# Optimization experiments

Measured on AMD Instinct MI355X. Metric: run time of the kernel, lower is better.

## Reference

```python
import jax, jax.numpy as jnp
import numpy as np

# Static block node counts (src of layer l has N[l] nodes, dst has N[l+1])
N = [100000, 50000, 25000, 12500]
E = [750000, 250000, 125000]
D = 128          # in_feats == n_hidden
E_PAIR = 10000   # pos/neg pair-graph edges
BN_EPS = 1e-5


def setup_inputs() -> dict:
    key = jax.random.key(0)
    ks = jax.random.split(key, 32)
    inp = {}
    inp['x'] = jax.random.normal(ks[0], (N[0], D), dtype=jnp.float32)
    for l in range(3):
        inp[f'src{l}'] = jax.random.randint(ks[1 + 2 * l], (E[l],), 0, N[l], dtype=jnp.int32)
        inp[f'dst{l}'] = jax.random.randint(ks[2 + 2 * l], (E[l],), 0, N[l + 1], dtype=jnp.int32)
    inp['perm'] = jax.random.permutation(ks[7], N[0]).astype(jnp.int32)
    inp['pos_src'] = jax.random.randint(ks[8], (E_PAIR,), 0, N[3], dtype=jnp.int32)
    inp['pos_dst'] = jax.random.randint(ks[9], (E_PAIR,), 0, N[3], dtype=jnp.int32)
    inp['neg_src'] = jax.random.randint(ks[10], (E_PAIR,), 0, N[3], dtype=jnp.int32)
    inp['neg_dst'] = jax.random.randint(ks[11], (E_PAIR,), 0, N[3], dtype=jnp.int32)
    s = 1.0 / np.sqrt(D)
    ki = 12
    for l in range(3):
        inp[f'Wself{l}'] = jax.random.normal(ks[ki], (D, D), dtype=jnp.float32) * s; ki += 1
        inp[f'Wneigh{l}'] = jax.random.normal(ks[ki], (D, D), dtype=jnp.float32) * s; ki += 1
        inp[f'b{l}'] = jnp.zeros((D,), dtype=jnp.float32)
    for l in range(2):
        inp[f'gamma{l}'] = jnp.ones((D,), dtype=jnp.float32)
        inp[f'beta{l}'] = jnp.zeros((D,), dtype=jnp.float32)
    inp['disc_W'] = jax.random.uniform(ks[ki], (D, D), dtype=jnp.float32, minval=-s, maxval=s); ki += 1
    inp['pW1'] = jax.random.normal(ks[ki], (D, D), dtype=jnp.float32) * s; ki += 1
    inp['pb1'] = jnp.zeros((D,), dtype=jnp.float32)
    inp['pW2'] = jax.random.normal(ks[ki], (D, D), dtype=jnp.float32) * s; ki += 1
    inp['pb2'] = jnp.zeros((D,), dtype=jnp.float32)
    inp['pW3'] = jax.random.normal(ks[ki], (D, 1), dtype=jnp.float32) * s; ki += 1
    inp['pb3'] = jnp.zeros((1,), dtype=jnp.float32)
    return inp


def _sage(h, src, dst, n_dst, Wself, Wneigh, b):
    # DGL SAGEConv('mean'): fc_self(h_dst) + fc_neigh(mean over in-neighbors)
    agg = jax.ops.segment_sum(h[src], dst, num_segments=n_dst)          # [n_dst, D]
    deg = jax.ops.segment_sum(jnp.ones(src.shape, h.dtype), dst, num_segments=n_dst)
    mean = agg / jnp.clip(deg, 1.0)[:, None]
    return h[:n_dst] @ Wself + mean @ Wneigh + b


def _bn(h, g, b):
    m = h.mean(0)
    v = h.var(0)
    return g * (h - m) * jax.lax.rsqrt(v + BN_EPS) + b


def _encode(h, blocks, params):
    for l in range(3):
        src, dst, n_dst = blocks[l]
        Ws, Wn, b, g, be = params[l]
        h = _sage(h, src, dst, n_dst, Ws, Wn, b)
        if l != 2:
            h = jax.nn.relu(_bn(h, g, be))  # dropout rate 0
    return h


def reference(x, src0, dst0, src1, dst1, src2, dst2, perm,
              pos_src, pos_dst, neg_src, neg_dst,
              Wself0, Wneigh0, b0, Wself1, Wneigh1, b1, Wself2, Wneigh2, b2,
              gamma0, beta0, gamma1, beta1, disc_W,
              pW1, pb1, pW2, pb2, pW3, pb3):
    blocks = [(src0, dst0, N[1]), (src1, dst1, N[2]), (src2, dst2, N[3])]
    params = [(Wself0, Wneigh0, b0, gamma0, beta0),
              (Wself1, Wneigh1, b1, gamma1, beta1),
              (Wself2, Wneigh2, b2, None, None)]
    positive = _encode(x, blocks, params)          # [N3, D]
    negative = _encode(x[perm], blocks, params)    # corruption: permuted features
    summary = jax.nn.sigmoid(positive.mean(0))     # [D]
    ws = disc_W @ summary                          # [D]
    pos = positive @ ws                            # [N3]
    neg = negative @ ws
    l1 = jnp.mean(jax.nn.softplus(-pos))           # BCEWithLogits vs ones
    l2 = jnp.mean(jax.nn.softplus(neg))            # BCEWithLogits vs zeros

    def predictor(z):
        z = jax.nn.relu(z @ pW1 + pb1)
        z = jax.nn.relu(z @ pW2 + pb2)
        return z @ pW3 + pb3

    h_pos = predictor(positive[pos_src] * positive[pos_dst])  # [E_PAIR, 1]
    h_neg = predictor(positive[neg_src] * positive[neg_dst])
    return h_pos, h_neg, l1 + l2
```

## Files before the change

kernel.cpp:

```cpp
#include <hip/hip_runtime.h>
#include <hip/hip_bf16.h>

#define DD 128
#define BN_EPS 1e-5f
#define NBLK 160

typedef __hip_bfloat16 bf16;
typedef __attribute__((ext_vector_type(8))) short short8;
typedef __attribute__((ext_vector_type(4))) float f32x4;

__device__ __forceinline__ float b2f(unsigned short u) {
    union { float f; unsigned int i; } x; x.i = ((unsigned int)u) << 16; return x.f;
}
__device__ __forceinline__ unsigned short f2bs(float v) {
    bf16 h = __float2bfloat16(v);
    return *(unsigned short*)&h;
}

__global__ void detect_dtype(const unsigned int* __restrict__ x, int* __restrict__ flag) {
    __shared__ int s[256];
    int t = threadIdx.x;
    unsigned int u = x[t];
    unsigned int e = (u >> 7) & 0xFFu;
    s[t] = ((e >= 90u && e <= 140u) || ((u & 0xFFFFu) == 0u)) ? 1 : 0;
    __syncthreads();
    for (int off = 128; off > 0; off >>= 1) { if (t < off) s[t] += s[t + off]; __syncthreads(); }
    if (t == 0) *flag = (s[0] >= 128) ? 1 : 0;
}

struct CvtTable {
    const void* src[20];
    int off[20];
    int n[20];
    int total;
};
__global__ __launch_bounds__(256) void cvt_all(CvtTable tab, float* __restrict__ wsf,
                                               const int* __restrict__ flagp) {
    int i = blockIdx.x * 256 + threadIdx.x;
    if (i >= tab.total) return;
    int k = 0;
    while (i >= tab.n[k]) { i -= tab.n[k]; ++k; }
    float v;
    if (*flagp) v = b2f(((const unsigned short*)tab.src[k])[i]);
    else        v = ((const float*)tab.src[k])[i];
    wsf[tab.off[k] + i] = v;
}

struct WfAll {
    const float* W1[5];
    const float* W2[5];
    unsigned short* dst[5];
    int KS[5];
    int start[5];
    int total;
};
__global__ __launch_bounds__(256) void wfrag_all(WfAll w) {
    int t = blockIdx.x * 256 + threadIdx.x;
    if (t >= w.total) return;
    int k = 0;
    while (k < 4 && t >= w.start[k + 1]) ++k;
    int lt = t - w.start[k];
    int KS = w.KS[k];
    int lane = lt & 63;
    int ks = (lt >> 6) % KS;
    int ct = lt / (KS * 64);
    int n = ct * 16 + (lane & 15);
    unsigned short v[8];
#pragma unroll
    for (int j = 0; j < 8; ++j) {
        int kk = ks * 32 + ((lane >> 4) & 3) * 8 + j;
        float wv = (kk < 128) ? w.W1[k][kk * DD + n] : w.W2[k][(kk - 128) * DD + n];
        v[j] = f2bs(wv);
    }
    *(uint4*)&w.dst[k][(size_t)lt * 8] = *(uint4*)v;
}

__global__ __launch_bounds__(256) void hist_win(
    const int* __restrict__ d0, int e0, const int* __restrict__ d1, int e1,
    const int* __restrict__ d2, int e2, int* __restrict__ hist) {
    int stride = gridDim.x * 256;
    int t0 = blockIdx.x * 256 + threadIdx.x;
    for (int w = 0; w < 4; ++w) {
        int dlo = w * 12500, dhi = dlo + 12500;
        for (int e = t0; e < e0; e += stride) {
            int d = d0[e];
            if (d >= dlo && d < dhi) atomicAdd(&hist[d], 1);
        }
    }
    for (int e = t0; e < e1; e += stride) atomicAdd(&hist[50000 + d1[e]], 1);
    for (int e = t0; e < e2; e += stride) atomicAdd(&hist[75000 + d2[e]], 1);
}

__global__ __launch_bounds__(256) void scan_bsum(const int* __restrict__ cnt, int n,
                                                 int* __restrict__ bsums) {
    __shared__ int sm[256];
    int t = threadIdx.x, b = blockIdx.x;
    int i4 = b * 256 + t;
    int local = 0;
    if (i4 * 4 < n) { int4 v = ((const int4*)cnt)[i4]; local = v.x + v.y + v.z + v.w; }
    sm[t] = local;
    __syncthreads();
    for (int off = 128; off > 0; off >>= 1) { if (t < off) sm[t] += sm[t + off]; __syncthreads(); }
    if (t == 0) bsums[b] = sm[0];
}
__global__ void scan_bscan(int* __restrict__ bsums, int nb, int* __restrict__ rowptr_n) {
    __shared__ int wsum[4];
    int t = threadIdx.x, lane = t & 63, w = t >> 6;
    int v = (t < nb) ? bsums[t] : 0;
    int inc = v;
    for (int off = 1; off < 64; off <<= 1) {
        int u = __shfl_up(inc, off, 64);
        if (lane >= off) inc += u;
    }
    if (lane == 63) wsum[w] = inc;
    __syncthreads();
    int wo = 0;
    for (int i = 0; i < w; ++i) wo += wsum[i];
    if (t < nb) bsums[t] = wo + inc - v;
    if (t == 255) *rowptr_n = wo + inc;
}
__global__ __launch_bounds__(256) void scan_apply(const int* __restrict__ cnt, int n,
                                                  const int* __restrict__ bsums,
                                                  int* __restrict__ rowptr) {
    __shared__ int wsum[4];
    int t = threadIdx.x, b = blockIdx.x, lane = t & 63, w = t >> 6;
    int i4 = b * 256 + t;
    int4 v = {0, 0, 0, 0};
    bool valid = (i4 * 4 < n);
    if (valid) v = ((const int4*)cnt)[i4];
    int local = v.x + v.y + v.z + v.w;
    int inc = local;
    for (int off = 1; off < 64; off <<= 1) {
        int u = __shfl_up(inc, off, 64);
        if (lane >= off) inc += u;
    }
    if (lane == 63) wsum[w] = inc;
    __syncthreads();
    int wo = 0;
    for (int i = 0; i < w; ++i) wo += wsum[i];
    if (valid) {
        int acc = bsums[b] + wo + inc - local;
        int base = i4 * 4;
        rowptr[base + 0] = acc; acc += v.x;
        rowptr[base + 1] = acc; acc += v.y;
        rowptr[base + 2] = acc; acc += v.z;
        rowptr[base + 3] = acc;
    }
}

__global__ __launch_bounds__(256) void csr_fill_win(
    const int* __restrict__ s0, const int* __restrict__ d0, int e0,
    const int* __restrict__ s1, const int* __restrict__ d1, int e1,
    const int* __restrict__ s2, const int* __restrict__ d2, int e2,
    const int* __restrict__ rpAll, int* __restrict__ cur, int* __restrict__ eid) {
    int stride = gridDim.x * 256;
    int t0 = blockIdx.x * 256 + threadIdx.x;
    for (int w = 0; w < 4; ++w) {
        int dlo = w * 12500, dhi = dlo + 12500;
        for (int e = t0; e < e0; e += stride) {
            int d = d0[e];
            if (d >= dlo && d < dhi)
                eid[rpAll[d] + atomicAdd(&cur[d], 1)] = s0[e];
        }
    }
    for (int e = t0; e < e1; e += stride) {
        int gd = 50000 + d1[e];
        eid[rpAll[gd] + atomicAdd(&cur[gd], 1)] = s1[e];
    }
    for (int e = t0; e < e2; e += stride) {
        int gd = 75000 + d2[e];
        eid[rpAll[gd] + atomicAdd(&cur[gd], 1)] = s2[e];
    }
}

__global__ __launch_bounds__(256) void gather2(
    const void* __restrict__ hvP, const void* __restrict__ hvN,
    const int* __restrict__ flagp,
    const int* __restrict__ permP, const int* __restrict__ permN,
    const float* __restrict__ scP, const float* __restrict__ shP,
    const float* __restrict__ scN, const float* __restrict__ shN,
    const int* __restrict__ rowptr, const int* __restrict__ eid,
    int N, int nRows, unsigned short* __restrict__ out)
{
    int row = blockIdx.x * 4 + (threadIdx.x >> 6);
    int lane = threadIdx.x & 63;
    if (row >= nRows) return;
    int half = row >= N;
    int d = half ? row - N : row;
    const void* hv = half ? hvN : hvP;
    const int* perm = half ? permN : permP;
    const float* sc = half ? scN : scP;
    const float* sh = half ? shN : shP;
    int i0 = rowptr[d], i1 = rowptr[d + 1];
    int abf = flagp ? *flagp : 1;
    bool bn = (sc != nullptr);
    float c0 = 1.0f, c1 = 1.0f, h0 = 0.0f, h1 = 0.0f;
    if (bn) { c0 = sc[lane * 2]; c1 = sc[lane * 2 + 1]; h0 = sh[lane * 2]; h1 = sh[lane * 2 + 1]; }

#define XF0(v) (bn ? fmaxf(c0 * (v) + h0, 0.0f) : (v))
#define XF1(v) (bn ? fmaxf(c1 * (v) + h1, 0.0f) : (v))
    float a0x = 0, a0y = 0, a1x = 0, a1y = 0, a2x = 0, a2y = 0, a3x = 0, a3y = 0;
    int i = i0;
    if (abf) {
        const unsigned short* h = (const unsigned short*)hv;
        for (; i + 4 <= i1; i += 4) {
            int s0 = eid[i], s1 = eid[i + 1], s2 = eid[i + 2], s3 = eid[i + 3];
            if (perm) { s0 = perm[s0]; s1 = perm[s1]; s2 = perm[s2]; s3 = perm[s3]; }
            ushort2 v0 = *(const ushort2*)&h[(size_t)s0 * DD + lane * 2];
            ushort2 v1 = *(const ushort2*)&h[(size_t)s1 * DD + lane * 2];
            ushort2 v2 = *(const ushort2*)&h[(size_t)s2 * DD + lane * 2];
            ushort2 v3 = *(const ushort2*)&h[(size_t)s3 * DD + lane * 2];
            a0x += XF0(b2f(v0.x)); a0y += XF1(b2f(v0.y));
            a1x += XF0(b2f(v1.x)); a1y += XF1(b2f(v1.y));
            a2x += XF0(b2f(v2.x)); a2y += XF1(b2f(v2.y));
            a3x += XF0(b2f(v3.x)); a3y += XF1(b2f(v3.y));
        }
        for (; i < i1; ++i) {
            int s = eid[i];
            if (perm) s = perm[s];
            ushort2 v = *(const ushort2*)&h[(size_t)s * DD + lane * 2];
            a0x += XF0(b2f(v.x)); a0y += XF1(b2f(v.y));
        }
    } else {
        const float* h = (const float*)hv;
        for (; i + 4 <= i1; i += 4) {
            int s0 = eid[i], s1 = eid[i + 1], s2 = eid[i + 2], s3 = eid[i + 3];
            if (perm) { s0 = perm[s0]; s1 = perm[s1]; s2 = perm[s2]; s3 = perm[s3]; }
            float2 v0 = *(const float2*)&h[(size_t)s0 * DD + lane * 2];
            float2 v1 = *(const float2*)&h[(size_t)s1 * DD + lane * 2];
            float2 v2 = *(const float2*)&h[(size_t)s2 * DD + lane * 2];
            float2 v3 = *(const float2*)&h[(size_t)s3 * DD + lane * 2];
            a0x += XF0(v0.x); a0y += XF1(v0.y);
            a1x += XF0(v1.x); a1y += XF1(v1.y);
            a2x += XF0(v2.x); a2y += XF1(v2.y);
            a3x += XF0(v3.x); a3y += XF1(v3.y);
        }
        for (; i < i1; ++i) {
            int s = eid[i];
            if (perm) s = perm[s];
            float2 v = *(const float2*)&h[(size_t)s * DD + lane * 2];
            a0x += XF0(v.x); a0y += XF1(v.y);
        }
    }
#undef XF0
#undef XF1
    float rd = 1.0f / fmaxf((float)(i1 - i0), 1.0f);
    ushort2 o;
    o.x = f2bs((a0x + a1x + a2x + a3x) * rd);
    o.y = f2bs((a0y + a1y + a2y + a3y) * rd);
    *(ushort2*)&out[(size_t)row * DD + lane * 2] = o;
}

#define ALD 264
__global__ __launch_bounds__(256) void mfma_gemm(
    const void* __restrict__ A1v, const int* __restrict__ flagp,
    const int* __restrict__ gather,
    const float* __restrict__ bnSc, const float* __restrict__ bnSh,
    const unsigned short* __restrict__ A2,
    const uint4* __restrict__ wfrag, const float* __restrict__ bias,
    unsigned short* __restrict__ out, int Mc, int relu,
    float* __restrict__ PSo, float* __restrict__ PQo)
{
    __shared__ unsigned short As[64 * ALD];
    __shared__ float sds[256];
    const int tid = threadIdx.x;
    const int rb = blockIdx.x * 64;
    const int abf = flagp ? *flagp : 1;
    const int KS = A2 ? 8 : 4;

    {
        int r = tid >> 2, cs = (tid & 3) * 32;
        int gr = rb + r;
        unsigned short* dst = &As[r * ALD + cs];
        if (gr < Mc) {
            int ar = gather ? gather[gr] : gr;
            if (abf) {
                if (bnSc) {
                    const unsigned short* s = (const unsigned short*)A1v + (size_t)ar * DD + cs;
#pragma unroll
                    for (int i = 0; i < 32; ++i) {
                        float v = b2f(s[i]);
                        v = fmaxf(bnSc[cs + i] * v + bnSh[cs + i], 0.0f);
                        dst[i] = f2bs(v);
                    }
                } else {
                    const uint4* s = (const uint4*)((const unsigned short*)A1v + (size_t)ar * DD + cs);
                    uint4* dv = (uint4*)dst;
#pragma unroll
                    for (int i = 0; i < 4; ++i) dv[i] = s[i];
                }
            } else {
                const float* s = (const float*)A1v + (size_t)ar * DD + cs;
#pragma unroll
                for (int i = 0; i < 32; ++i) dst[i] = f2bs(s[i]);
            }
            if (A2) {
                const uint4* s2 = (const uint4*)(A2 + (size_t)gr * DD + cs);
                uint4* d2 = (uint4*)(dst + 128);
#pragma unroll
                for (int i = 0; i < 4; ++i) d2[i] = s2[i];
            }
        } else {
            uint4 z = {0, 0, 0, 0};
            uint4* dv = (uint4*)dst;
#pragma unroll
            for (int i = 0; i < 4; ++i) dv[i] = z;
            if (A2) {
                uint4* d2 = (uint4*)(dst + 128);
#pragma unroll
                for (int i = 0; i < 4; ++i) d2[i] = z;
            }
        }
    }
    if (PSo) { sds[tid] = 0.0f; }
    __syncthreads();

    const int w = tid >> 6, lane = tid & 63;
    const int m0 = w * 16;
    f32x4 acc[8] = {};

    for (int ks = 0; ks < KS; ++ks) {
        short8 a = *(const short8*)&As[(m0 + (lane & 15)) * ALD + ks * 32 + ((lane >> 4) & 3) * 8];
#pragma unroll
        for (int ct = 0; ct < 8; ++ct) {
            uint4 braw = wfrag[(ct * KS + ks) * 64 + lane];
            short8 b = *(short8*)&braw;
            acc[ct] = __builtin_amdgcn_mfma_f32_16x16x32_bf16(a, b, acc[ct], 0, 0, 0);
        }
    }

#pragma unroll
    for (int ct = 0; ct < 8; ++ct) {
        int col = ct * 16 + (lane & 15);
        float bv = bias[col];
        float sv = 0.0f, sq = 0.0f;
#pragma unroll
        for (int r = 0; r < 4; ++r) {
            int grow = rb + m0 + ((lane >> 4) & 3) * 4 + r;
            float v = acc[ct][r] + bv;
            if (relu) v = fmaxf(v, 0.0f);
            if (grow < Mc) {
                out[(size_t)grow * DD + col] = f2bs(v);
                sv += v; sq += v * v;
            }
        }
        if (PSo) {
            sv += __shfl_down(sv, 32, 64); sv += __shfl_down(sv, 16, 64);
            sq += __shfl_down(sq, 32, 64); sq += __shfl_down(sq, 16, 64);
            if (lane < 16) {
                atomicAdd(&sds[ct * 16 + lane], sv);
                atomicAdd(&sds[128 + ct * 16 + lane], sq);
            }
        }
    }
    if (PSo) {
        __syncthreads();
        if (tid < 128) {
            PSo[blockIdx.x * 128 + tid] = sds[tid];
            PQo[blockIdx.x * 128 + tid] = sds[128 + tid];
        }
    }
}

__global__ __launch_bounds__(256) void p2bn_fast(
    const float* __restrict__ PSa, const float* __restrict__ PQa,
    float* __restrict__ sca, float* __restrict__ sha,
    const float* __restrict__ PSb, const float* __restrict__ PQb,
    float* __restrict__ scb, float* __restrict__ shb,
    int nb, int M,
    const float* __restrict__ gamma, const float* __restrict__ beta)
{
    int tensor = blockIdx.x >> 7, col = blockIdx.x & 127;
    const float* PS = tensor ? PSb : PSa;
    const float* PQ = tensor ? PQb : PQa;
    float* sc = tensor ? scb : sca;
    float* sh = tensor ? shb : sha;
    __shared__ float sS[256], sQ[256];
    int t = threadIdx.x;
    float s = 0.0f, q = 0.0f;
    for (int b = t; b < nb; b += 256) {
        s += PS[b * 128 + col];
        q += PQ[b * 128 + col];
    }
    sS[t] = s; sQ[t] = q;
    __syncthreads();
    for (int off = 128; off > 0; off >>= 1) {
        if (t < off) { sS[t] += sS[t + off]; sQ[t] += sQ[t + off]; }
        __syncthreads();
    }
    if (t == 0) {
        float m = sS[0] / (float)M;
        float var = fmaxf(sQ[0] / (float)M - m * m, 0.0f);
        float inv = rsqrtf(var + BN_EPS);
        float g = gamma[col];
        sc[col] = g * inv;
        sh[col] = beta[col] - g * m * inv;
    }
}

__global__ __launch_bounds__(256) void colreduce(const float* __restrict__ PS, int nb,
                                                 float* __restrict__ out) {
    __shared__ float sS[256];
    int col = blockIdx.x;
    int t = threadIdx.x;
    float s = 0.0f;
    for (int b = t; b < nb; b += 256) s += PS[b * 128 + col];
    sS[t] = s;
    __syncthreads();
    for (int off = 128; off > 0; off >>= 1) { if (t < off) sS[t] += sS[t + off]; __syncthreads(); }
    if (t == 0) out[col] = sS[0];
}

__global__ void make_ws(const float* __restrict__ colsum, const float* __restrict__ discW,
                        float* __restrict__ wsv, int M) {
    __shared__ float s[128];
    int t = threadIdx.x;
    s[t] = 1.0f / (1.0f + expf(-(colsum[t] / (float)M)));
    __syncthreads();
    float acc = 0.0f;
#pragma unroll
    for (int j = 0; j < 128; ++j) acc += discW[t * 128 + j] * s[j];
    wsv[t] = acc;
}

__global__ __launch_bounds__(256) void loss_partial(
    const unsigned short* __restrict__ P, const unsigned short* __restrict__ Ng,
    const float* __restrict__ wsv, float* __restrict__ lossP, float* __restrict__ lossN, int M)
{
    __shared__ float sP[4], sN[4];
    int lane = threadIdx.x & 63;
    int wave = threadIdx.x >> 6;
    int gw = blockIdx.x * 4 + wave;
    int nw = gridDim.x * 4;
    float w0 = wsv[lane], w1 = wsv[lane + 64];
    float accP = 0.0f, accN = 0.0f;
    for (int row = gw; row < 2 * M; row += nw) {
        const unsigned short* base = (row < M) ? &P[(size_t)row * DD]
                                               : &Ng[(size_t)(row - M) * DD];
        float a = b2f(base[lane]) * w0 + b2f(base[lane + 64]) * w1;
#pragma unroll
        for (int off = 32; off > 0; off >>= 1) a += __shfl_down(a, off, 64);
        if (lane == 0) {
            float x = (row < M) ? -a : a;
            float sp = fmaxf(x, 0.0f) + log1pf(expf(-fabsf(x)));
            if (row < M) accP += sp; else accN += sp;
        }
    }
    if (lane == 0) { sP[wave] = accP; sN[wave] = accN; }
    __syncthreads();
    if (threadIdx.x == 0) {
        lossP[blockIdx.x] = sP[0] + sP[1] + sP[2] + sP[3];
        lossN[blockIdx.x] = sN[0] + sN[1] + sN[2] + sN[3];
    }
}

__global__ void write_loss(const float* __restrict__ lossP, const float* __restrict__ lossN,
                           void* __restrict__ outv, int M, const int* __restrict__ flagp) {
    __shared__ float s[256];
    int t = threadIdx.x;
    s[t] = (t < NBLK) ? (lossP[t] + lossN[t]) : 0.0f;
    __syncthreads();
    for (int off = 128; off > 0; off >>= 1) { if (t < off) s[t] += s[t + off]; __syncthreads(); }
    if (t == 0) {
        float v = s[0] / (float)M;
        if (*flagp) ((bf16*)outv)[20000] = __float2bfloat16(v);
        else        ((float*)outv)[20000] = v;
    }
}

__global__ __launch_bounds__(256) void pair_mult(
    const unsigned short* __restrict__ P,
    const int* __restrict__ ps, const int* __restrict__ pd,
    const int* __restrict__ ns, const int* __restrict__ nd,
    unsigned short* __restrict__ Z, int nPair) {
    int i = blockIdx.x * 2 + (threadIdx.x >> 7);
    int f = threadIdx.x & 127;
    if (i >= 2 * nPair) return;
    int a = (i < nPair) ? ps[i] : ns[i - nPair];
    int b = (i < nPair) ? pd[i] : nd[i - nPair];
    float v = b2f(P[(size_t)a * DD + f]) * b2f(P[(size_t)b * DD + f]);
    Z[(size_t)i * DD + f] = f2bs(v);
}

__global__ __launch_bounds__(256) void final_mv(
    const unsigned short* __restrict__ ZB, const float* __restrict__ pW3,
    const float* __restrict__ pb3,
    void* __restrict__ outv, int nRows, const int* __restrict__ flagp) {
    int row = blockIdx.x * 4 + (threadIdx.x >> 6);
    int lane = threadIdx.x & 63;
    if (row >= nRows) return;
    float a = b2f(ZB[(size_t)row * DD + lane]) * pW3[lane]
            + b2f(ZB[(size_t)row * DD + lane + 64]) * pW3[lane + 64];
#pragma unroll
    for (int off = 32; off > 0; off >>= 1) a += __shfl_down(a, off, 64);
    if (lane == 0) {
        float v = a + pb3[0];
        if (*flagp) ((bf16*)outv)[row] = __float2bfloat16(v);
        else        ((float*)outv)[row] = v;
    }
}

extern "C" void kernel_launch(void* const* d_in, const int* in_sizes, int n_in,
                              void* d_out, int out_size, void* d_ws, size_t ws_size,
                              hipStream_t stream)
{
    const void* x      = d_in[0];
    const int* srcA[3] = {(const int*)d_in[1], (const int*)d_in[3], (const int*)d_in[5]};
    const int* dstA[3] = {(const int*)d_in[2], (const int*)d_in[4], (const int*)d_in[6]};
    const int* perm    = (const int*)d_in[7];
    const int* pos_src = (const int*)d_in[8];
    const int* pos_dst = (const int*)d_in[9];
    const int* neg_src = (const int*)d_in[10];
    const int* neg_dst = (const int*)d_in[11];

    const int N1 = 50000, N2 = 25000, N3 = 12500;
    const int E[3] = {750000, 250000, 125000};
    const int EP = 10000;
    const int NCAT = 87500;

    float* wsf = (float*)d_ws;
    int*   wsi = (int*)d_ws;
    int*   flagp = wsi;
    float* lossP = wsf + 64;
    float* lossN = wsf + 224;
    float* wsvec = wsf + 512;
    float* scP0 = wsf + 640;  float* shP0 = wsf + 768;
    float* scN0 = wsf + 896;  float* shN0 = wsf + 1024;
    float* scP1 = wsf + 1152; float* shP1 = wsf + 1280;
    float* scN1 = wsf + 1408; float* shN1 = wsf + 1536;
    int*   bsums = wsi + 1664;
    float* colsum = wsf + 1920;
    float* PSP = wsf + 2048;
    float* PQP = wsf + 102400;
    float* PSN = wsf + 202752;
    float* PQN = wsf + 303104;
    int* histAll = wsi + 403456;
    int* curAll  = wsi + 491008;
    int* rpAll   = wsi + 578560;
    int* eidAll  = wsi + 666112;
    const size_t WfB = 1791232;
    float* WS[3] = {wsf + WfB, wsf + WfB + 32896, wsf + WfB + 65792};
    float* WN[3] = {wsf + WfB + 16384, wsf + WfB + 49280, wsf + WfB + 82176};
    float* BV[3] = {wsf + WfB + 32768, wsf + WfB + 65664, wsf + WfB + 98560};
    float* G0  = wsf + WfB + 98688;  float* BE0 = wsf + WfB + 98816;
    float* G1  = wsf + WfB + 98944;  float* BE1 = wsf + WfB + 99072;
    float* DW  = wsf + WfB + 99200;
    float* PW1 = wsf + WfB + 115584; float* PB1 = wsf + WfB + 131968;
    float* PW2 = wsf + WfB + 132096; float* PB2 = wsf + WfB + 148480;
    float* PW3 = wsf + WfB + 148608; float* PB3 = wsf + WfB + 148736;
    unsigned short* wfragL[3] = {(unsigned short*)(wsf + 1940480),
                                 (unsigned short*)(wsf + 1956864),
                                 (unsigned short*)(wsf + 1973248)};
    unsigned short* wfragP[2] = {(unsigned short*)(wsf + 1989632),
                                 (unsigned short*)(wsf + 1997824)};
    unsigned short* PF  = (unsigned short*)(wsf + 2006016);
    unsigned short* NF  = (unsigned short*)(wsf + 2806016);
    unsigned short* H2P = (unsigned short*)(wsf + 3606016);
    unsigned short* H2N = (unsigned short*)(wsf + 5206016);
    unsigned short* H1P = (unsigned short*)(wsf + 6806016);
    unsigned short* H1N = (unsigned short*)(wsf + 10006016);
    unsigned short* AGG = (unsigned short*)(wsf + 13206016);
    unsigned short* Z  = H1P;
    unsigned short* ZA = H1N;
    unsigned short* ZB = H1N + (size_t)1280000 * 2;

    detect_dtype<<<1, 256, 0, stream>>>((const unsigned int*)x, flagp);
    CvtTable tab;
    const int widx[20] = {12,13,14, 15,16,17, 18,19,20, 21,22,23,24, 25, 26,27, 28,29, 30,31};
    float* wdst[20] = {WS[0],WN[0],BV[0], WS[1],WN[1],BV[1], WS[2],WN[2],BV[2],
                       G0,BE0,G1,BE1, DW, PW1,PB1, PW2,PB2, PW3,PB3};
    const int wn[20] = {16384,16384,128, 16384,16384,128, 16384,16384,128,
                        128,128,128,128, 16384, 16384,128, 16384,128, 128,1};
    int tot = 0;
    for (int k = 0; k < 20; ++k) {
        tab.src[k] = d_in[widx[k]];
        tab.off[k] = (int)(wdst[k] - wsf);
        tab.n[k] = wn[k];
        tot += wn[k];
    }
    tab.total = tot;
    cvt_all<<<(tot + 255) / 256, 256, 0, stream>>>(tab, wsf, flagp);

    hipMemsetAsync(histAll, 0, (size_t)(2 * NCAT + 128) * 4, stream);
    hist_win<<<512, 256, 0, stream>>>(dstA[0], E[0], dstA[1], E[1], dstA[2], E[2], histAll);
    {
        int nb = (NCAT / 4 + 255) / 256;
        scan_bsum<<<nb, 256, 0, stream>>>(histAll, NCAT, bsums);
        scan_bscan<<<1, 256, 0, stream>>>(bsums, nb, rpAll + NCAT);
        scan_apply<<<nb, 256, 0, stream>>>(histAll, NCAT, bsums, rpAll);
    }
    csr_fill_win<<<512, 256, 0, stream>>>(
        srcA[0], dstA[0], E[0], srcA[1], dstA[1], E[1], srcA[2], dstA[2], E[2],
        rpAll, curAll, eidAll);

    WfAll wa;
    wa.W1[0] = WS[0]; wa.W2[0] = WN[0]; wa.dst[0] = wfragL[0]; wa.KS[0] = 8; wa.start[0] = 0;
    wa.W1[1] = WS[1]; wa.W2[1] = WN[1]; wa.dst[1] = wfragL[1]; wa.KS[1] = 8; wa.start[1] = 4096;
    wa.W1[2] = WS[2]; wa.W2[2] = WN[2]; wa.dst[2] = wfragL[2]; wa.KS[2] = 8; wa.start[2] = 8192;
    wa.W1[3] = PW1;   wa.W2[3] = nullptr; wa.dst[3] = wfragP[0]; wa.KS[3] = 4; wa.start[3] = 12288;
    wa.W1[4] = PW2;   wa.W2[4] = nullptr; wa.dst[4] = wfragP[1]; wa.KS[4] = 4; wa.start[4] = 14336;
    wa.total = 16384;
    wfrag_all<<<64, 256, 0, stream>>>(wa);

    const int nb0 = (N1 + 63) / 64, nb1 = (N2 + 63) / 64, nb2 = (N3 + 63) / 64;

    gather2<<<(N1 + 3) / 4, 256, 0, stream>>>(
        x, x, flagp, nullptr, nullptr, nullptr, nullptr, nullptr, nullptr,
        rpAll, eidAll, N1, N1, AGG);
    mfma_gemm<<<nb0, 256, 0, stream>>>(
        x, flagp, nullptr, nullptr, nullptr, AGG, (const uint4*)wfragL[0], BV[0],
        H1P, N1, 0, PSP, PQP);
    gather2<<<(N1 + 3) / 4, 256, 0, stream>>>(
        x, x, flagp, perm, perm, nullptr, nullptr, nullptr, nullptr,
        rpAll, eidAll, N1, N1, AGG);
    mfma_gemm<<<nb0, 256, 0, stream>>>(
        x, flagp, perm, nullptr, nullptr, AGG, (const uint4*)wfragL[0], BV[0],
        H1N, N1, 0, PSN, PQN);
    p2bn_fast<<<256, 256, 0, stream>>>(PSP, PQP, scP0, shP0, PSN, PQN, scN0, shN0, nb0, N1, G0, BE0);

    gather2<<<(2 * N2 + 3) / 4, 256, 0, stream>>>(
        H1P, H1N, nullptr, nullptr, nullptr, scP0, shP0, scN0, shN0,
        rpAll + 50000, eidAll, N2, 2 * N2, AGG);
    mfma_gemm<<<nb1, 256, 0, stream>>>(
        H1P, nullptr, nullptr, scP0, shP0, AGG, (const uint4*)wfragL[1], BV[1],
        H2P, N2, 0, PSP, PQP);
    mfma_gemm<<<nb1, 256, 0, stream>>>(
        H1N, nullptr, nullptr, scN0, shN0, AGG + (size_t)N2 * DD, (const uint4*)wfragL[1], BV[1],
        H2N, N2, 0, PSN, PQN);
    p2bn_fast<<<256, 256, 0, stream>>>(PSP, PQP, scP1, shP1, PSN, PQN, scN1, shN1, nb1, N2, G1, BE1);

    gather2<<<(2 * N3 + 3) / 4, 256, 0, stream>>>(
        H2P, H2N, nullptr, nullptr, nullptr, scP1, shP1, scN1, shN1,
        rpAll + 75000, eidAll, N3, 2 * N3, AGG);
    mfma_gemm<<<nb2, 256, 0, stream>>>(
        H2P, nullptr, nullptr, scP1, shP1, AGG, (const uint4*)wfragL[2], BV[2],
        PF, N3, 0, PSP, PQP);
    mfma_gemm<<<nb2, 256, 0, stream>>>(
        H2N, nullptr, nullptr, scN1, shN1, AGG + (size_t)N3 * DD, (const uint4*)wfragL[2], BV[2],
        NF, N3, 0, nullptr, nullptr);
    colreduce<<<128, 256, 0, stream>>>(PSP, nb2, colsum);
    make_ws<<<1, 128, 0, stream>>>(colsum, DW, wsvec, N3);

    loss_partial<<<NBLK, 256, 0, stream>>>(PF, NF, wsvec, lossP, lossN, N3);
    write_loss<<<1, 256, 0, stream>>>(lossP, lossN, d_out, N3, flagp);

    pair_mult<<<EP, 256, 0, stream>>>(PF, pos_src, pos_dst, neg_src, neg_dst, Z, EP);
    mfma_gemm<<<(2 * EP + 63) / 64, 256, 0, stream>>>(
        Z, nullptr, nullptr, nullptr, nullptr, nullptr, (const uint4*)wfragP[0], PB1,
        ZA, 2 * EP, 1, nullptr, nullptr);
    mfma_gemm<<<(2 * EP + 63) / 64, 256, 0, stream>>>(
        ZA, nullptr, nullptr, nullptr, nullptr, nullptr, (const uint4*)wfragP[1], PB2,
        ZB, 2 * EP, 1, nullptr, nullptr);
    final_mv<<<(2 * EP + 3) / 4, 256, 0, stream>>>(ZB, PW3, PB3, d_out, 2 * EP, flagp);
}
```

Baseline: 662.5 us.

## Fuse neighbor mean-aggregation into SAGE GEMM and merge pos/neg halves

Replaces the separate gather kernel plus the GEMM with a single sage_layer kernel that aggregates neighbor means straight into the shared-memory A tile, then runs the MFMA GEMM. Positive and negative encodings are handled in one launch by splitting the grid in half. The pair multiply is fused into the first predictor GEMM's load stage. This removes the AGG intermediate round trip to global memory and several launches. In exchange each block serializes 16 rows of gather per wave before the GEMM, which can reduce memory-level parallelism.

Measured after the change: 811.5 us. +22.5%, slower.

```diff
diff --git a/kernel.cpp b/kernel.cpp
--- a/kernel.cpp
+++ b/kernel.cpp
@@ -4,6 +4,8 @@
 #define DD 128
 #define BN_EPS 1e-5f
 #define NBLK 160
+#define ALD 264
+#define PLD 136
 
 typedef __hip_bfloat16 bf16;
 typedef __attribute__((ext_vector_type(8))) short short8;
@@ -173,157 +175,139 @@
     }
 }
 
-__global__ __launch_bounds__(256) void gather2(
-    const void* __restrict__ hvP, const void* __restrict__ hvN,
-    const int* __restrict__ flagp,
-    const int* __restrict__ permP, const int* __restrict__ permN,
-    const float* __restrict__ scP, const float* __restrict__ shP,
-    const float* __restrict__ scN, const float* __restrict__ shN,
+struct HalfArgs {
+    const void* base;
+    const int* perm;
+    const float* sc;
+    const float* sh;
+    unsigned short* out;
+    float* PS;
+    float* PQ;
+};
+__global__ __launch_bounds__(256) void sage_layer(
+    HalfArgs hP, HalfArgs hN, const int* __restrict__ flagp,
     const int* __restrict__ rowptr, const int* __restrict__ eid,
-    int N, int nRows, unsigned short* __restrict__ out)
-{
-    int row = blockIdx.x * 4 + (threadIdx.x >> 6);
-    int lane = threadIdx.x & 63;
-    if (row >= nRows) return;
-    int half = row >= N;
-    int d = half ? row - N : row;
-    const void* hv = half ? hvN : hvP;
-    const int* perm = half ? permN : permP;
-    const float* sc = half ? scN : scP;
-    const float* sh = half ? shN : shP;
-    int i0 = rowptr[d], i1 = rowptr[d + 1];
-    int abf = flagp ? *flagp : 1;
-    bool bn = (sc != nullptr);
-    float c0 = 1.0f, c1 = 1.0f, h0 = 0.0f, h1 = 0.0f;
-    if (bn) { c0 = sc[lane * 2]; c1 = sc[lane * 2 + 1]; h0 = sh[lane * 2]; h1 = sh[lane * 2 + 1]; }
-
-#define XF0(v) (bn ? fmaxf(c0 * (v) + h0, 0.0f) : (v))
-#define XF1(v) (bn ? fmaxf(c1 * (v) + h1, 0.0f) : (v))
-    float a0x = 0, a0y = 0, a1x = 0, a1y = 0, a2x = 0, a2y = 0, a3x = 0, a3y = 0;
-    int i = i0;
-    if (abf) {
-        const unsigned short* h = (const unsigned short*)hv;
-        for (; i + 4 <= i1; i += 4) {
-            int s0 = eid[i], s1 = eid[i + 1], s2 = eid[i + 2], s3 = eid[i + 3];
-            if (perm) { s0 = perm[s0]; s1 = perm[s1]; s2 = perm[s2]; s3 = perm[s3]; }
-            ushort2 v0 = *(const ushort2*)&h[(size_t)s0 * DD + lane * 2];
-            ushort2 v1 = *(const ushort2*)&h[(size_t)s1 * DD + lane * 2];
-            ushort2 v2 = *(const ushort2*)&h[(size_t)s2 * DD + lane * 2];
-            ushort2 v3 = *(const ushort2*)&h[(size_t)s3 * DD + lane * 2];
-            a0x += XF0(b2f(v0.x)); a0y += XF1(b2f(v0.y));
-            a1x += XF0(b2f(v1.x)); a1y += XF1(b2f(v1.y));
-            a2x += XF0(b2f(v2.x)); a2y += XF1(b2f(v2.y));
-            a3x += XF0(b2f(v3.x)); a3y += XF1(b2f(v3.y));
-        }
-        for (; i < i1; ++i) {
-            int s = eid[i];
-            if (perm) s = perm[s];
-            ushort2 v = *(const ushort2*)&h[(size_t)s * DD + lane * 2];
-            a0x += XF0(b2f(v.x)); a0y += XF1(b2f(v.y));
-        }
-    } else {
-        const float* h = (const float*)hv;
-        for (; i + 4 <= i1; i += 4) {
-            int s0 = eid[i], s1 = eid[i + 1], s2 = eid[i + 2], s3 = eid[i + 3];
-            if (perm) { s0 = perm[s0]; s1 = perm[s1]; s2 = perm[s2]; s3 = perm[s3]; }
-            float2 v0 = *(const float2*)&h[(size_t)s0 * DD + lane * 2];
-            float2 v1 = *(const float2*)&h[(size_t)s1 * DD + lane * 2];
-            float2 v2 = *(const float2*)&h[(size_t)s2 * DD + lane * 2];
-            float2 v3 = *(const float2*)&h[(size_t)s3 * DD + lane * 2];
-            a0x += XF0(v0.x); a0y += XF1(v0.y);
-            a1x += XF0(v1.x); a1y += XF1(v1.y);
-            a2x += XF0(v2.x); a2y += XF1(v2.y);
-            a3x += XF0(v3.x); a3y += XF1(v3.y);
-        }
-        for (; i < i1; ++i) {
-            int s = eid[i];
-            if (perm) s = perm[s];
-            float2 v = *(const float2*)&h[(size_t)s * DD + lane * 2];
-            a0x += XF0(v.x); a0y += XF1(v.y);
-        }
-    }
-#undef XF0
-#undef XF1
-    float rd = 1.0f / fmaxf((float)(i1 - i0), 1.0f);
-    ushort2 o;
-    o.x = f2bs((a0x + a1x + a2x + a3x) * rd);
-    o.y = f2bs((a0y + a1y + a2y + a3y) * rd);
-    *(ushort2*)&out[(size_t)row * DD + lane * 2] = o;
-}
-
-#define ALD 264
-__global__ __launch_bounds__(256) void mfma_gemm(
-    const void* __restrict__ A1v, const int* __restrict__ flagp,
-    const int* __restrict__ gather,
-    const float* __restrict__ bnSc, const float* __restrict__ bnSh,
-    const unsigned short* __restrict__ A2,
     const uint4* __restrict__ wfrag, const float* __restrict__ bias,
-    unsigned short* __restrict__ out, int Mc, int relu,
-    float* __restrict__ PSo, float* __restrict__ PQo)
+    int Nh, int nbHalf)
 {
     __shared__ unsigned short As[64 * ALD];
     __shared__ float sds[256];
     const int tid = threadIdx.x;
-    const int rb = blockIdx.x * 64;
+    const int half = blockIdx.x / nbHalf;
+    const int rb = (blockIdx.x % nbHalf) * 64;
+    const HalfArgs H = half ? hN : hP;
     const int abf = flagp ? *flagp : 1;
-    const int KS = A2 ? 8 : 4;
+    const bool bn = (H.sc != nullptr);
+    const bool doStats = (H.PS != nullptr);
 
     {
         int r = tid >> 2, cs = (tid & 3) * 32;
         int gr = rb + r;
         unsigned short* dst = &As[r * ALD + cs];
-        if (gr < Mc) {
-            int ar = gather ? gather[gr] : gr;
+        if (gr < Nh) {
+            int ar = H.perm ? H.perm[gr] : gr;
             if (abf) {
-                if (bnSc) {
-                    const unsigned short* s = (const unsigned short*)A1v + (size_t)ar * DD + cs;
+                const unsigned short* s = (const unsigned short*)H.base + (size_t)ar * DD + cs;
+                if (bn) {
 #pragma unroll
                     for (int i = 0; i < 32; ++i) {
                         float v = b2f(s[i]);
-                        v = fmaxf(bnSc[cs + i] * v + bnSh[cs + i], 0.0f);
+                        v = fmaxf(H.sc[cs + i] * v + H.sh[cs + i], 0.0f);
                         dst[i] = f2bs(v);
                     }
                 } else {
-                    const uint4* s = (const uint4*)((const unsigned short*)A1v + (size_t)ar * DD + cs);
+                    const uint4* sv = (const uint4*)s;
                     uint4* dv = (uint4*)dst;
 #pragma unroll
-                    for (int i = 0; i < 4; ++i) dv[i] = s[i];
+                    for (int i = 0; i < 4; ++i) dv[i] = sv[i];
                 }
             } else {
-                const float* s = (const float*)A1v + (size_t)ar * DD + cs;
+                const float* s = (const float*)H.base + (size_t)ar * DD + cs;
 #pragma unroll
                 for (int i = 0; i < 32; ++i) dst[i] = f2bs(s[i]);
-            }
-            if (A2) {
-                const uint4* s2 = (const uint4*)(A2 + (size_t)gr * DD + cs);
-                uint4* d2 = (uint4*)(dst + 128);
-#pragma unroll
-                for (int i = 0; i < 4; ++i) d2[i] = s2[i];
             }
         } else {
             uint4 z = {0, 0, 0, 0};
             uint4* dv = (uint4*)dst;
 #pragma unroll
             for (int i = 0; i < 4; ++i) dv[i] = z;
-            if (A2) {
-                uint4* d2 = (uint4*)(dst + 128);
-#pragma unroll
-                for (int i = 0; i < 4; ++i) d2[i] = z;
-            }
-        }
-    }
-    if (PSo) { sds[tid] = 0.0f; }
-    __syncthreads();
+        }
+    }
 
     const int w = tid >> 6, lane = tid & 63;
+
+    float c0 = 1.0f, c1 = 1.0f, h0 = 0.0f, h1 = 0.0f;
+    if (bn) { c0 = H.sc[lane * 2]; c1 = H.sc[lane * 2 + 1];
+              h0 = H.sh[lane * 2]; h1 = H.sh[lane * 2 + 1]; }
+#define XF0(v) (bn ? fmaxf(c0 * (v) + h0, 0.0f) : (v))
+#define XF1(v) (bn ? fmaxf(c1 * (v) + h1, 0.0f) : (v))
+    for (int j = 0; j < 16; ++j) {
+        int r = w * 16 + j;
+        int d = rb + r;
+        unsigned short* dst2 = &As[r * ALD + 128 + lane * 2];
+        if (d >= Nh) { ushort2 z = {0, 0}; *(ushort2*)dst2 = z; continue; }
+        int i0 = rowptr[d], i1 = rowptr[d + 1];
+        float a0x = 0, a0y = 0, a1x = 0, a1y = 0, a2x = 0, a2y = 0, a3x = 0, a3y = 0;
+        int i = i0;
+        if (abf) {
+            const unsigned short* h = (const unsigned short*)H.base;
+            for (; i + 4 <= i1; i += 4) {
+                int s0 = eid[i], s1 = eid[i + 1], s2 = eid[i + 2], s3 = eid[i + 3];
+                if (H.perm) { s0 = H.perm[s0]; s1 = H.perm[s1]; s2 = H.perm[s2]; s3 = H.perm[s3]; }
+                ushort2 v0 = *(const ushort2*)&h[(size_t)s0 * DD + lane * 2];
+                ushort2 v1 = *(const ushort2*)&h[(size_t)s1 * DD + lane * 2];
+                ushort2 v2 = *(const ushort2*)&h[(size_t)s2 * DD + lane * 2];
+                ushort2 v3 = *(const ushort2*)&h[(size_t)s3 * DD + lane * 2];
+                a0x += XF0(b2f(v0.x)); a0y += XF1(b2f(v0.y));
+                a1x += XF0(b2f(v1.x)); a1y += XF1(b2f(v1.y));
+                a2x += XF0(b2f(v2.x)); a2y += XF1(b2f(v2.y));
+                a3x += XF0(b2f(v3.x)); a3y += XF1(b2f(v3.y));
+            }
+            for (; i < i1; ++i) {
+                int s = eid[i];
+                if (H.perm) s = H.perm[s];
+                ushort2 v = *(const ushort2*)&h[(size_t)s * DD + lane * 2];
+                a0x += XF0(b2f(v.x)); a0y += XF1(b2f(v.y));
+            }
+        } else {
+            const float* h = (const float*)H.base;
+            for (; i + 4 <= i1; i += 4) {
+                int s0 = eid[i], s1 = eid[i + 1], s2 = eid[i + 2], s3 = eid[i + 3];
+                if (H.perm) { s0 = H.perm[s0]; s1 = H.perm[s1]; s2 = H.perm[s2]; s3 = H.perm[s3]; }
+                float2 v0 = *(const float2*)&h[(size_t)s0 * DD + lane * 2];
+                float2 v1 = *(const float2*)&h[(size_t)s1 * DD + lane * 2];
+                float2 v2 = *(const float2*)&h[(size_t)s2 * DD + lane * 2];
+                float2 v3 = *(const float2*)&h[(size_t)s3 * DD + lane * 2];
+                a0x += XF0(v0.x); a0y += XF1(v0.y);
+                a1x += XF0(v1.x); a1y += XF1(v1.y);
+                a2x += XF0(v2.x); a2y += XF1(v2.y);
+                a3x += XF0(v3.x); a3y += XF1(v3.y);
+            }
+            for (; i < i1; ++i) {
+                int s = eid[i];
+                if (H.perm) s = H.perm[s];
+                float2 v = *(const float2*)&h[(size_t)s * DD + lane * 2];
+                a0x += XF0(v.x); a0y += XF1(v.y);
+            }
+        }
+        float rd = 1.0f / fmaxf((float)(i1 - i0), 1.0f);
+        ushort2 o;
+        o.x = f2bs((a0x + a1x + a2x + a3x) * rd);
+        o.y = f2bs((a0y + a1y + a2y + a3y) * rd);
+        *(ushort2*)dst2 = o;
+    }
+#undef XF0
+#undef XF1
+
+    if (doStats) { sds[tid] = 0.0f; __syncthreads(); }
+
     const int m0 = w * 16;
     f32x4 acc[8] = {};
-
-    for (int ks = 0; ks < KS; ++ks) {
+    for (int ks = 0; ks < 8; ++ks) {
         short8 a = *(const short8*)&As[(m0 + (lane & 15)) * ALD + ks * 32 + ((lane >> 4) & 3) * 8];
 #pragma unroll
         for (int ct = 0; ct < 8; ++ct) {
-            uint4 braw = wfrag[(ct * KS + ks) * 64 + lane];
+            uint4 braw = wfrag[(ct * 8 + ks) * 64 + lane];
             short8 b = *(short8*)&braw;
             acc[ct] = __builtin_amdgcn_mfma_f32_16x16x32_bf16(a, b, acc[ct], 0, 0, 0);
         }
@@ -338,13 +322,12 @@
         for (int r = 0; r < 4; ++r) {
             int grow = rb + m0 + ((lane >> 4) & 3) * 4 + r;
             float v = acc[ct][r] + bv;
-            if (relu) v = fmaxf(v, 0.0f);
-            if (grow < Mc) {
-                out[(size_t)grow * DD + col] = f2bs(v);
+            if (grow < Nh) {
+                H.out[(size_t)grow * DD + col] = f2bs(v);
                 sv += v; sq += v * v;
             }
         }
-        if (PSo) {
+        if (doStats) {
             sv += __shfl_down(sv, 32, 64); sv += __shfl_down(sv, 16, 64);
             sq += __shfl_down(sq, 32, 64); sq += __shfl_down(sq, 16, 64);
             if (lane < 16) {
@@ -353,11 +336,77 @@
             }
         }
     }
-    if (PSo) {
+    if (doStats) {
         __syncthreads();
         if (tid < 128) {
-            PSo[blockIdx.x * 128 + tid] = sds[tid];
-            PQo[blockIdx.x * 128 + tid] = sds[128 + tid];
+            H.PS[(blockIdx.x % nbHalf) * 128 + tid] = sds[tid];
+            H.PQ[(blockIdx.x % nbHalf) * 128 + tid] = sds[128 + tid];
+        }
+    }
+}
+
+__global__ __launch_bounds__(256) void pred_gemm(
+    const unsigned short* __restrict__ A,
+    const unsigned short* __restrict__ PF,
+    const int* __restrict__ ps, const int* __restrict__ pd,
+    const int* __restrict__ ns, const int* __restrict__ nd, int EPc,
+    const uint4* __restrict__ wfrag, const float* __restrict__ bias,
+    unsigned short* __restrict__ out, int Mc)
+{
+    __shared__ unsigned short As[64 * PLD];
+    const int tid = threadIdx.x;
+    const int rb = blockIdx.x * 64;
+
+    {
+        int r = tid >> 2, cs = (tid & 3) * 32;
+        int gr = rb + r;
+        unsigned short* dst = &As[r * PLD + cs];
+        if (gr < Mc) {
+            if (ps) {
+                int a = (gr < EPc) ? ps[gr] : ns[gr - EPc];
+                int b = (gr < EPc) ? pd[gr] : nd[gr - EPc];
+                const unsigned short* ra = PF + (size_t)a * DD + cs;
+                const unsigned short* rbp = PF + (size_t)b * DD + cs;
+#pragma unroll
+                for (int i = 0; i < 32; ++i)
+                    dst[i] = f2bs(b2f(ra[i]) * b2f(rbp[i]));
+            } else {
+                const uint4* sv = (const uint4*)(A + (size_t)gr * DD + cs);
+                uint4* dv = (uint4*)dst;
+#pragma unroll
+                for (int i = 0; i < 4; ++i) dv[i] = sv[i];
+            }
+        } else {
+            uint4 z = {0, 0, 0, 0};
+            uint4* dv = (uint4*)dst;
+#pragma unroll
+            for (int i = 0; i < 4; ++i) dv[i] = z;
+        }
+    }
+
+    const int w = tid >> 6, lane = tid & 63;
+    const int m0 = w * 16;
+    f32x4 acc[8] = {};
+    for (int ks = 0; ks < 4; ++ks) {
+        short8 a = *(const short8*)&As[(m0 + (lane & 15)) * PLD + ks * 32 + ((lane >> 4) & 3) * 8];
+#pragma unroll
+        for (int ct = 0; ct < 8; ++ct) {
+            uint4 braw = wfrag[(ct * 4 + ks) * 64 + lane];
+            short8 b = *(short8*)&braw;
+            acc[ct] = __builtin_amdgcn_mfma_f32_16x16x32_bf16(a, b, acc[ct], 0, 0, 0);
+        }
+    }
+
+#pragma unroll
+    for (int ct = 0; ct < 8; ++ct) {
+        int col = ct * 16 + (lane & 15);
+        float bv = bias[col];
+#pragma unroll
+        for (int r = 0; r < 4; ++r) {
+            int grow = rb + m0 + ((lane >> 4) & 3) * 4 + r;
+            if (grow >= Mc) continue;
+            float v = fmaxf(acc[ct][r] + bv, 0.0f);
+            out[(size_t)grow * DD + col] = f2bs(v);
         }
     }
 }
@@ -466,20 +515,6 @@
         if (*flagp) ((bf16*)outv)[20000] = __float2bfloat16(v);
         else        ((float*)outv)[20000] = v;
     }
-}
-
-__global__ __launch_bounds__(256) void pair_mult(
-    const unsigned short* __restrict__ P,
-    const int* __restrict__ ps, const int* __restrict__ pd,
-    const int* __restrict__ ns, const int* __restrict__ nd,
-    unsigned short* __restrict__ Z, int nPair) {
-    int i = blockIdx.x * 2 + (threadIdx.x >> 7);
-    int f = threadIdx.x & 127;
-    if (i >= 2 * nPair) return;
-    int a = (i < nPair) ? ps[i] : ns[i - nPair];
-    int b = (i < nPair) ? pd[i] : nd[i - nPair];
-    float v = b2f(P[(size_t)a * DD + f]) * b2f(P[(size_t)b * DD + f]);
-    Z[(size_t)i * DD + f] = f2bs(v);
 }
 
 __global__ __launch_bounds__(256) void final_mv(
@@ -559,10 +594,8 @@
     unsigned short* H2N = (unsigned short*)(wsf + 5206016);
     unsigned short* H1P = (unsigned short*)(wsf + 6806016);
     unsigned short* H1N = (unsigned short*)(wsf + 10006016);
-    unsigned short* AGG = (unsigned short*)(wsf + 13206016);
-    unsigned short* Z  = H1P;
     unsigned short* ZA = H1N;
-    unsigned short* ZB = H1N + (size_t)1280000 * 2;
+    unsigned short* ZB = H1N + (size_t)2560000;
 
     detect_dtype<<<1, 256, 0, stream>>>((const unsigned int*)x, flagp);
     CvtTable tab;
@@ -604,52 +637,39 @@
 
     const int nb0 = (N1 + 63) / 64, nb1 = (N2 + 63) / 64, nb2 = (N3 + 63) / 64;
 
-    gather2<<<(N1 + 3) / 4, 256, 0, stream>>>(
-        x, x, flagp, nullptr, nullptr, nullptr, nullptr, nullptr, nullptr,
-        rpAll, eidAll, N1, N1, AGG);
-    mfma_gemm<<<nb0, 256, 0, stream>>>(
-        x, flagp, nullptr, nullptr, nullptr, AGG, (const uint4*)wfragL[0], BV[0],
-        H1P, N1, 0, PSP, PQP);
-    gather2<<<(N1 + 3) / 4, 256, 0, stream>>>(
-        x, x, flagp, perm, perm, nullptr, nullptr, nullptr, nullptr,
-        rpAll, eidAll, N1, N1, AGG);
-    mfma_gemm<<<nb0, 256, 0, stream>>>(
-        x, flagp, perm, nullptr, nullptr, AGG, (const uint4*)wfragL[0], BV[0],
-        H1N, N1, 0, PSN, PQN);
+    {
+        HalfArgs hP = {x, nullptr, nullptr, nullptr, H1P, PSP, PQP};
+        HalfArgs hN = {x, perm,    nullptr, nullptr, H1N, PSN, PQN};
+        sage_layer<<<2 * nb0, 256, 0, stream>>>(hP, hN, flagp, rpAll, eidAll,
+                                                (const uint4*)wfragL[0], BV[0], N1, nb0);
+    }
     p2bn_fast<<<256, 256, 0, stream>>>(PSP, PQP, scP0, shP0, PSN, PQN, scN0, shN0, nb0, N1, G0, BE0);
 
-    gather2<<<(2 * N2 + 3) / 4, 256, 0, stream>>>(
-        H1P, H1N, nullptr, nullptr, nullptr, scP0, shP0, scN0, shN0,
-        rpAll + 50000, eidAll, N2, 2 * N2, AGG);
-    mfma_gemm<<<nb1, 256, 0, stream>>>(
-        H1P, nullptr, nullptr, scP0, shP0, AGG, (const uint4*)wfragL[1], BV[1],
-        H2P, N2, 0, PSP, PQP);
-    mfma_gemm<<<nb1, 256, 0, stream>>>(
-        H1N, nullptr, nullptr, scN0, shN0, AGG + (size_t)N2 * DD, (const uint4*)wfragL[1], BV[1],
-        H2N, N2, 0, PSN, PQN);
+    {
+        HalfArgs hP = {H1P, nullptr, scP0, shP0, H2P, PSP, PQP};
+        HalfArgs hN = {H1N, nullptr, scN0, shN0, H2N, PSN, PQN};
+        sage_layer<<<2 * nb1, 256, 0, stream>>>(hP, hN, nullptr, rpAll + 50000, eidAll,
+                                                (const uint4*)wfragL[1], BV[1], N2, nb1);
+    }
     p2bn_fast<<<256, 256, 0, stream>>>(PSP, PQP, scP1, shP1, PSN, PQN, scN1, shN1, nb1, N2, G1, BE1);
 
-    gather2<<<(2 * N3 + 3) / 4, 256, 0, stream>>>(
-        H2P, H2N, nullptr, nullptr, nullptr, scP1, shP1, scN1, shN1,
-        rpAll + 75000, eidAll, N3, 2 * N3, AGG);
-    mfma_gemm<<<nb2, 256, 0, stream>>>(
-        H2P, nullptr, nullptr, scP1, shP1, AGG, (const uint4*)wfragL[2], BV[2],
-        PF, N3, 0, PSP, PQP);
-    mfma_gemm<<<nb2, 256, 0, stream>>>(
-        H2N, nullptr, nullptr, scN1, shN1, AGG + (size_t)N3 * DD, (const uint4*)wfragL[2], BV[2],
-        NF, N3, 0, nullptr, nullptr);
+    {
+        HalfArgs hP = {H2P, nullptr, scP1, shP1, PF, PSP, PQP};
+        HalfArgs hN = {H2N, nullptr, scN1, shN1, NF, nullptr, nullptr};
+        sage_layer<<<2 * nb2, 256, 0, stream>>>(hP, hN, nullptr, rpAll + 75000, eidAll,
+                                                (const uint4*)wfragL[2], BV[2], N3, nb2);
+    }
     colreduce<<<128, 256, 0, stream>>>(PSP, nb2, colsum);
     make_ws<<<1, 128, 0, stream>>>(colsum, DW, wsvec, N3);
 
     loss_partial<<<NBLK, 256, 0, stream>>>(PF, NF, wsvec, lossP, lossN, N3);
     write_loss<<<1, 256, 0, stream>>>(lossP, lossN, d_out, N3, flagp);
 
-    pair_mult<<<EP, 256, 0, stream>>>(PF, pos_src, pos_dst, neg_src, neg_dst, Z, EP);
-    mfma_gemm<<<(2 * EP + 63) / 64, 256, 0, stream>>>(
-        Z, nullptr, nullptr, nullptr, nullptr, nullptr, (const uint4*)wfragP[0], PB1,
-        ZA, 2 * EP, 1, nullptr, nullptr);
-    mfma_gemm<<<(2 * EP + 63) / 64, 256, 0, stream>>>(
-        ZA, nullptr, nullptr, nullptr, nullptr, nullptr, (const uint4*)wfragP[1], PB2,
-        ZB, 2 * EP, 1, nullptr, nullptr);
+    pred_gemm<<<(2 * EP + 63) / 64, 256, 0, stream>>>(
+        nullptr, PF, pos_src, pos_dst, neg_src, neg_dst, EP,
+        (const uint4*)wfragP[0], PB1, ZA, 2 * EP);
+    pred_gemm<<<(2 * EP + 63) / 64, 256, 0, stream>>>(
+        ZA, nullptr, nullptr, nullptr, nullptr, nullptr, 0,
+        (const uint4*)wfragP[1], PB2, ZB, 2 * EP);
     final_mv<<<(2 * EP + 3) / 4, 256, 0, stream>>>(ZB, PW3, PB3, d_out, 2 * EP, flagp);
 }
```
